# Performance work log

Measured on AMD Instinct MI355X. Metric: run time of the kernel, lower is better.

The kernel has to match this reference:

```python
import math
import jax, jax.numpy as jnp
import numpy as np

EMBED_DIM = 1024
NUM_HEADS = 16
FACTOR = 5


def setup_inputs() -> dict:
    key = jax.random.key(0)
    kx, kw, kb, kow, kob = jax.random.split(key, 5)
    B, S, E = 8, 4096, EMBED_DIM
    scale = 1.0 / math.sqrt(E)
    x = jax.random.normal(kx, (B, S, E), dtype=jnp.float32)
    # nn.MultiheadAttention params: packed in_proj (q,k,v) and out_proj
    in_proj_w = jax.random.uniform(kw, (3 * E, E), dtype=jnp.float32, minval=-scale, maxval=scale)
    in_proj_b = jnp.zeros((3 * E,), dtype=jnp.float32)
    out_w = jax.random.uniform(kow, (E, E), dtype=jnp.float32, minval=-scale, maxval=scale)
    out_b = jnp.zeros((E,), dtype=jnp.float32)
    return {"x": x, "in_proj_w": in_proj_w, "in_proj_b": in_proj_b, "out_w": out_w, "out_b": out_b}


def reference(x, in_proj_w, in_proj_b, out_w, out_b):
    B, S, E = x.shape
    H = NUM_HEADS
    hd = E // H
    k = max(1, int(FACTOR * math.log(S + 1)))
    k = min(k, S)

    # top-k queries by L2 norm of each token
    energy = jnp.linalg.norm(x, axis=-1)            # [B, S]
    _, topk_idx = jax.lax.top_k(energy, k)          # [B, k]

    q_tok = jnp.take_along_axis(x, topk_idx[..., None], axis=1)  # [B, k, E]

    Wq, Wk, Wv = jnp.split(in_proj_w, 3, axis=0)    # each [E, E]
    bq, bk, bv = jnp.split(in_proj_b, 3, axis=0)

    q = (q_tok @ Wq.T + bq).reshape(B, k, H, hd)    # [B, k, H, hd]
    kk = (x @ Wk.T + bk).reshape(B, S, H, hd)       # [B, S, H, hd]
    v = (x @ Wv.T + bv).reshape(B, S, H, hd)

    scores = jnp.einsum("bqhd,bshd->bhqs", q, kk) / math.sqrt(hd)
    attn = jax.nn.softmax(scores, axis=-1)          # [B, H, k, S]
    ctx = jnp.einsum("bhqs,bshd->bqhd", attn, v).reshape(B, k, E)
    out_sel = ctx @ out_w.T + out_b                 # [B, k, E]

    # default value for non-selected positions: per-batch mean of x
    default = jnp.mean(x, axis=1)                   # [B, E]
    result = jnp.broadcast_to(default[:, None, :], (B, S, E))
    batch_ar = jnp.arange(B)[:, None]
    result = result.at[batch_ar, topk_idx].set(out_sel)
    return result
```

## Files before the change

kernel.cpp:

```cpp
#include <hip/hip_runtime.h>

using u16 = unsigned short;
using u32 = unsigned int;
using u64 = unsigned long long;
typedef __attribute__((ext_vector_type(8))) short s16x8;
typedef __attribute__((ext_vector_type(4))) short s16x4;
typedef __attribute__((ext_vector_type(4))) float f32x4;

__device__ __forceinline__ float bf2f(u16 u){ return __uint_as_float(((u32)u)<<16); }
__device__ __forceinline__ u16 f2bf(float f){
  u32 u = __float_as_uint(f);
  u += 0x7fffu + ((u>>16)&1u);
  return (u16)(u>>16);
}
__device__ __forceinline__ void gl_lds16(const void* g, void* l){
  __builtin_amdgcn_global_load_lds((const __attribute__((address_space(1))) void*)g,
                                   (__attribute__((address_space(3))) void*)l, 16, 0, 0);
}

__global__ __launch_bounds__(256) void k_cvt(const float* __restrict__ in, u16* __restrict__ outp, int n){
  int i = (blockIdx.x*256 + threadIdx.x)*4;
  if (i >= n) return;
  float4 v = *(const float4*)(in + i);
  s16x4 o;
  o[0]=(short)f2bf(v.x); o[1]=(short)f2bf(v.y); o[2]=(short)f2bf(v.z); o[3]=(short)f2bf(v.w);
  *(s16x4*)(outp + i) = o;
}

__global__ __launch_bounds__(256) void k_prep_x(const float* __restrict__ x, u16* __restrict__ xb, float* __restrict__ energy){
  int tok = blockIdx.x*4 + (threadIdx.x>>6);
  int lane = threadIdx.x & 63;
  const float* p = x + (size_t)tok*1024 + lane*16;
  float4 a[4];
  #pragma unroll
  for (int j=0;j<4;++j) a[j] = ((const float4*)p)[j];
  float s = 0.f;
  s16x8 o0, o1;
  #pragma unroll
  for (int j=0;j<2;++j){
    o0[j*4+0]=(short)f2bf(a[j].x); o0[j*4+1]=(short)f2bf(a[j].y);
    o0[j*4+2]=(short)f2bf(a[j].z); o0[j*4+3]=(short)f2bf(a[j].w);
  }
  #pragma unroll
  for (int j=0;j<2;++j){
    o1[j*4+0]=(short)f2bf(a[2+j].x); o1[j*4+1]=(short)f2bf(a[2+j].y);
    o1[j*4+2]=(short)f2bf(a[2+j].z); o1[j*4+3]=(short)f2bf(a[2+j].w);
  }
  #pragma unroll
  for (int j=0;j<4;++j){
    s += a[j].x*a[j].x + a[j].y*a[j].y + a[j].z*a[j].z + a[j].w*a[j].w;
  }
  u16* xo = xb + (size_t)tok*1024 + lane*16;
  *(s16x8*)xo = o0;
  *(s16x8*)(xo+8) = o1;
  #pragma unroll
  for (int off=32; off; off>>=1) s += __shfl_xor(s, off);
  if (lane==0) energy[tok] = s;
}

__global__ __launch_bounds__(256) void k_colsum(const u16* __restrict__ xb, float* __restrict__ colsum){
  int b = blockIdx.x, sc = blockIdx.y;
  int t = threadIdx.x;
  float acc[4] = {0.f,0.f,0.f,0.f};
  for (int s = sc*128; s < sc*128+128; ++s){
    s16x4 v = *(const s16x4*)(xb + ((size_t)b*4096 + s)*1024 + t*4);
    #pragma unroll
    for (int i=0;i<4;++i) acc[i] += bf2f((u16)v[i]);
  }
  #pragma unroll
  for (int i=0;i<4;++i) atomicAdd(&colsum[b*1024 + t*4 + i], acc[i]);
}

__global__ __launch_bounds__(256) void k_topk(const float* __restrict__ energy, int* __restrict__ topk, int* __restrict__ sel){
  int b = blockIdx.x, t = threadIdx.x;
  int lane = t & 63, wid = t >> 6;
  __shared__ u64 wmax[4];
  __shared__ u64 winner;
  u64 v[16];
  #pragma unroll
  for (int i=0;i<16;++i){
    u32 tok = i*256 + t;
    float e = energy[b*4096 + tok];
    v[i] = ((u64)__float_as_uint(e) << 32) | (u32)(~tok);
    sel[b*4096 + tok] = -1;
  }
  __syncthreads();
  for (int it=0; it<41; ++it){
    u64 m = v[0];
    #pragma unroll
    for (int i=1;i<16;++i) m = v[i] > m ? v[i] : m;
    #pragma unroll
    for (int off=32; off; off>>=1){
      u64 o = __shfl_xor(m, off);
      m = o > m ? o : m;
    }
    if (lane==0) wmax[wid] = m;
    __syncthreads();
    if (t==0){
      u64 g = wmax[0];
      #pragma unroll
      for (int w=1;w<4;++w) g = wmax[w] > g ? wmax[w] : g;
      winner = g;
      u32 tok = (~(u32)g) & 4095u;
      topk[b*64+it] = (int)tok;
      sel[b*4096 + tok] = it;
    }
    __syncthreads();
    u32 wtok = (~(u32)winner) & 4095u;
    #pragma unroll
    for (int i=0;i<16;++i){
      if ((u32)(i*256 + t) == wtok) v[i] = 0;
    }
  }
}

__global__ __launch_bounds__(256) void k_gather_q(const float* __restrict__ x, const int* __restrict__ topk,
                                                  u16* __restrict__ Aq){
  int b = blockIdx.x, qi = blockIdx.y, t = threadIdx.x;
  size_t dst = ((size_t)(b*48+qi))*1024 + t*4;
  if (qi >= 41){ s16x4 z = {0,0,0,0}; *(s16x4*)&Aq[dst] = z; return; }
  int tok = topk[b*64+qi];
  float4 v = *(const float4*)(x + ((size_t)b*4096 + tok)*1024 + t*4);
  s16x4 o;
  o[0]=(short)f2bf(v.x); o[1]=(short)f2bf(v.y); o[2]=(short)f2bf(v.z); o[3]=(short)f2bf(v.w);
  *(s16x4*)&Aq[dst] = o;
}

__global__ __launch_bounds__(256) void k_gemm(const u16* __restrict__ A, const u16* __restrict__ Bk,
                                              const u16* __restrict__ Bv,
                                              const u16* __restrict__ biask, const u16* __restrict__ biasv,
                                              u16* __restrict__ C, int nbn, int ncols, int half, float cscale){
  __shared__ u16 As[128*64];
  __shared__ u16 Bs[128*64];
  const int tid = threadIdx.x;
  const int bn = blockIdx.x % nbn;
  const int bm = blockIdx.x / nbn;
  const int m0 = bm*128, n0 = bn*128;
  const u16* Bbase  = (n0 < half) ? (Bk + (size_t)n0*1024) : (Bv + (size_t)(n0-half)*1024);
  const u16* biasp  = (n0 < half) ? (biask + n0) : (biasv + (n0-half));
  const int lane = tid & 63;
  const int wave = tid >> 6;
  const int wr = wave >> 1, wc = wave & 1;
  const int fr = lane & 15;
  const int fq = lane >> 4;
  f32x4 acc[4][4] = {};
  for (int k0 = 0; k0 < 1024; k0 += 64){
    __syncthreads();
    #pragma unroll
    for (int j=0;j<4;++j){
      int idx = j*256 + tid;
      int r = idx>>3; int cc = (idx&7)*8;
      gl_lds16(A + (size_t)(m0+r)*1024 + k0 + cc, &As[r*64+cc]);
    }
    #pragma unroll
    for (int j=0;j<4;++j){
      int idx = j*256 + tid;
      int r = idx>>3; int cc = (idx&7)*8;
      gl_lds16(Bbase + (size_t)r*1024 + k0 + cc, &Bs[r*64+cc]);
    }
    __syncthreads();
    #pragma unroll
    for (int kk=0; kk<64; kk+=32){
      s16x8 af[4], bfv[4];
      #pragma unroll
      for (int m=0;m<4;++m) af[m] = *(const s16x8*)&As[(wr*64 + m*16 + fr)*64 + kk + fq*8];
      #pragma unroll
      for (int n=0;n<4;++n) bfv[n] = *(const s16x8*)&Bs[(wc*64 + n*16 + fr)*64 + kk + fq*8];
      #pragma unroll
      for (int m=0;m<4;++m)
        #pragma unroll
        for (int n=0;n<4;++n)
          acc[m][n] = __builtin_amdgcn_mfma_f32_16x16x32_bf16(af[m], bfv[n], acc[m][n], 0,0,0);
    }
  }
  #pragma unroll
  for (int n=0;n<4;++n){
    int cl = wc*64 + n*16 + fr;
    int col = n0 + cl;
    float bvv = bf2f(biasp[cl]);
    #pragma unroll
    for (int m=0;m<4;++m){
      int rowb = m0 + wr*64 + m*16 + fq*4;
      f32x4 v = acc[m][n];
      #pragma unroll
      for (int i=0;i<4;++i)
        C[(size_t)(rowb+i)*ncols + col] = f2bf((v[i]+bvv)*cscale);
    }
  }
}

__device__ __forceinline__ void stageA2(const u16* __restrict__ A, int m0, int k0, u16* ldsSlot, int tid){
  #pragma unroll
  for (int j=0;j<4;++j){
    int idx = j*512 + tid;
    int row = idx>>3;
    int chunk = (tid&7) ^ (row&7);
    gl_lds16(A + (size_t)(m0+row)*1024 + k0 + chunk*8, ldsSlot + (size_t)idx*8);
  }
}
__device__ __forceinline__ void stageB2(const u16* __restrict__ B, int k0, u16* ldsSlot, int tid){
  #pragma unroll
  for (int j=0;j<2;++j){
    int idx = j*512 + tid;
    int row = idx>>3;
    int chunk = (tid&7) ^ (row&7);
    gl_lds16(B + (size_t)row*1024 + k0 + chunk*8, ldsSlot + 16384 + (size_t)idx*8);
  }
}
__device__ __forceinline__ s16x8 fragA2(const u16* slot, int row, int k2, int fq){
  int chunk = (fq + k2*4) ^ (row&7);
  return *(const s16x8*)(slot + row*64 + chunk*8);
}
__device__ __forceinline__ s16x8 fragB2(const u16* slot, int row, int k2, int fq){
  int chunk = (fq + k2*4) ^ (row&7);
  return *(const s16x8*)(slot + 16384 + row*64 + chunk*8);
}

__global__ __launch_bounds__(512) void k_kvgemm2(const u16* __restrict__ A, const u16* __restrict__ Bk,
                                                 const u16* __restrict__ Bv,
                                                 const u16* __restrict__ biask, const u16* __restrict__ biasv,
                                                 u16* __restrict__ C){
  __shared__ u16 lds[3*24576];
  const int tid = threadIdx.x;
  const int bn = blockIdx.x & 15;
  const int bm = blockIdx.x >> 4;
  const int m0 = bm*256, n0 = bn*128;
  const u16* Bbase = (bn < 8) ? (Bk + (size_t)n0*1024) : (Bv + (size_t)(n0-1024)*1024);
  const u16* biasp = (bn < 8) ? (biask + n0) : (biasv + (n0-1024));
  const int lane = tid & 63, wid = tid >> 6;
  const int wm = wid >> 1, wn = wid & 1;
  const int fr = lane & 15, fq = lane >> 4;
  f32x4 acc[4][4] = {};

  stageA2(A, m0, 0, lds, tid);        stageB2(Bbase, 0, lds, tid);
  stageA2(A, m0, 64, lds+24576, tid); stageB2(Bbase, 64, lds+24576, tid);
  asm volatile("s_waitcnt vmcnt(6)" ::: "memory");
  __builtin_amdgcn_sched_barrier(0);
  __builtin_amdgcn_s_barrier();
  __builtin_amdgcn_sched_barrier(0);

  for (int t=0; t<16; ++t){
    const u16* slot = lds + (t%3)*24576;
    u16* nslot = (u16*)lds + ((t+2)%3)*24576;
    s16x8 afr[4][2], bfr[2][2];
    #pragma unroll
    for (int m=0;m<4;++m)
      #pragma unroll
      for (int k2=0;k2<2;++k2)
        afr[m][k2] = fragA2(slot, wm*64 + m*16 + fr, k2, fq);
    #pragma unroll
    for (int n=0;n<2;++n)
      #pragma unroll
      for (int k2=0;k2<2;++k2)
        bfr[n][k2] = fragB2(slot, wn*64 + n*16 + fr, k2, fq);
    if (t < 14) stageA2(A, m0, (t+2)*64, nslot, tid);
    __builtin_amdgcn_sched_barrier(0);
    __builtin_amdgcn_s_barrier();
    __builtin_amdgcn_sched_barrier(0);
    __builtin_amdgcn_s_setprio(1);
    #pragma unroll
    for (int m=0;m<4;++m)
      #pragma unroll
      for (int n=0;n<2;++n)
        #pragma unroll
        for (int k2=0;k2<2;++k2)
          acc[m][n] = __builtin_amdgcn_mfma_f32_16x16x32_bf16(afr[m][k2], bfr[n][k2], acc[m][n], 0,0,0);
    __builtin_amdgcn_s_setprio(0);
    __builtin_amdgcn_sched_barrier(0);
    __builtin_amdgcn_s_barrier();
    __builtin_amdgcn_sched_barrier(0);
    #pragma unroll
    for (int n=0;n<2;++n)
      #pragma unroll
      for (int k2=0;k2<2;++k2)
        bfr[n][k2] = fragB2(slot, wn*64 + (n+2)*16 + fr, k2, fq);
    if (t < 14) stageB2(Bbase, (t+2)*64, nslot, tid);
    __builtin_amdgcn_sched_barrier(0);
    __builtin_amdgcn_s_setprio(1);
    #pragma unroll
    for (int m=0;m<4;++m)
      #pragma unroll
      for (int n=0;n<2;++n)
        #pragma unroll
        for (int k2=0;k2<2;++k2)
          acc[m][n+2] = __builtin_amdgcn_mfma_f32_16x16x32_bf16(afr[m][k2], bfr[n][k2], acc[m][n+2], 0,0,0);
    __builtin_amdgcn_s_setprio(0);
    if (t < 14){
      asm volatile("s_waitcnt vmcnt(6)" ::: "memory");
    } else if (t == 14){
      asm volatile("s_waitcnt vmcnt(0)" ::: "memory");
    }
    __builtin_amdgcn_sched_barrier(0);
    __builtin_amdgcn_s_barrier();
    __builtin_amdgcn_sched_barrier(0);
  }

  #pragma unroll
  for (int n=0;n<4;++n){
    int cl = wn*64 + n*16 + fr;
    int col = n0 + cl;
    float bvv = bf2f(biasp[cl]);
    #pragma unroll
    for (int m=0;m<4;++m){
      int rowb = m0 + wm*64 + m*16 + fq*4;
      f32x4 v = acc[m][n];
      #pragma unroll
      for (int i=0;i<4;++i)
        C[(size_t)(rowb+i)*2048 + col] = f2bf(v[i]+bvv);
    }
  }
}

__global__ __launch_bounds__(64) void k_attn(const u16* __restrict__ qb, const u16* __restrict__ KV,
                                             float* __restrict__ part_ctx, float* __restrict__ part_ml,
                                             int G, int hg0, int ncols, int half, int nt, int NSP){
  const int b = blockIdx.x / G, hl = blockIdx.x % G;
  const int h = hg0 + hl;
  const int bh = b*16 + h;
  const int sp = blockIdx.y;
  const int lane = threadIdx.x;
  const int fr = lane & 15, fq = lane >> 4;
  __shared__ u16 k_lds[64*72];
  __shared__ u16 v_lds[64*72];
  __shared__ u16 p_lds[48*72];
  s16x8 af[3][2];
  #pragma unroll
  for (int m=0;m<3;++m)
    #pragma unroll
    for (int kk=0;kk<2;++kk)
      af[m][kk] = *(const s16x8*)(qb + ((size_t)(b*48 + m*16 + fr))*1024 + h*64 + kk*32 + fq*8);
  f32x4 acc_o[3][4] = {};
  float m_run[3][4], l_run[3][4];
  #pragma unroll
  for (int m=0;m<3;++m)
    #pragma unroll
    for (int i=0;i<4;++i){ m_run[m][i] = -3e38f; l_run[m][i] = 0.f; }

  for (int it=0; it<nt; ++it){
    int s0 = (sp*nt + it)*64;
    __syncthreads();
    #pragma unroll
    for (int j=0;j<8;++j){
      int r = j*8 + (lane>>3);
      int sg = (lane&7)*8;
      const u16* kp = KV + ((size_t)(b*4096 + s0 + r))*ncols + hl*64 + sg;
      *(s16x8*)&k_lds[r*72+sg] = *(const s16x8*)kp;
      *(s16x8*)&v_lds[r*72+sg] = *(const s16x8*)(kp+half);
    }
    __syncthreads();
    f32x4 sc4[3][4] = {};
    #pragma unroll
    for (int kk=0;kk<2;++kk){
      s16x8 bk[4];
      #pragma unroll
      for (int n=0;n<4;++n)
        bk[n] = *(const s16x8*)&k_lds[(n*16+fr)*72 + kk*32 + fq*8];
      #pragma unroll
      for (int m=0;m<3;++m)
        #pragma unroll
        for (int n=0;n<4;++n)
          sc4[m][n] = __builtin_amdgcn_mfma_f32_16x16x32_bf16(af[m][kk], bk[n], sc4[m][n], 0,0,0);
    }
    #pragma unroll
    for (int m=0;m<3;++m){
      #pragma unroll
      for (int i=0;i<4;++i){
        float rmax = fmaxf(fmaxf(sc4[m][0][i], sc4[m][1][i]), fmaxf(sc4[m][2][i], sc4[m][3][i]));
        #pragma unroll
        for (int off=1; off<16; off<<=1) rmax = fmaxf(rmax, __shfl_xor(rmax, off));
        float mnew = fmaxf(m_run[m][i], rmax);
        float alpha = __expf(m_run[m][i] - mnew);
        m_run[m][i] = mnew;
        float rsum = 0.f;
        #pragma unroll
        for (int n=0;n<4;++n){
          float p = __expf(sc4[m][n][i] - mnew);
          rsum += p;
          p_lds[(m*16 + fq*4 + i)*72 + n*16 + fr] = f2bf(p);
        }
        #pragma unroll
        for (int off=1; off<16; off<<=1) rsum += __shfl_xor(rsum, off);
        l_run[m][i] = l_run[m][i]*alpha + rsum;
        #pragma unroll
        for (int n=0;n<4;++n) acc_o[m][n][i] *= alpha;
      }
    }
    __syncthreads();
    #pragma unroll
    for (int kk=0;kk<2;++kk){
      s16x8 ap[3];
      #pragma unroll
      for (int m=0;m<3;++m)
        ap[m] = *(const s16x8*)&p_lds[(m*16+fr)*72 + kk*32 + fq*8];
      #pragma unroll
      for (int n=0;n<4;++n){
        s16x8 bv;
        #pragma unroll
        for (int i2=0;i2<8;++i2)
          bv[i2] = (short)v_lds[(kk*32 + fq*8 + i2)*72 + n*16 + fr];
        #pragma unroll
        for (int m=0;m<3;++m)
          acc_o[m][n] = __builtin_amdgcn_mfma_f32_16x16x32_bf16(ap[m], bv, acc_o[m][n], 0,0,0);
      }
    }
  }
  size_t pbase = ((size_t)(bh*NSP + sp))*48*64;
  #pragma unroll
  for (int m=0;m<3;++m)
    #pragma unroll
    for (int n=0;n<4;++n)
      #pragma unroll
      for (int i=0;i<4;++i){
        int qi = m*16 + fq*4 + i, d = n*16 + fr;
        part_ctx[pbase + (size_t)qi*64 + d] = acc_o[m][n][i];
      }
  if (fr==0){
    #pragma unroll
    for (int m=0;m<3;++m)
      #pragma unroll
      for (int i=0;i<4;++i){
        int qi = m*16 + fq*4 + i;
        part_ml[((size_t)(bh*NSP+sp))*96 + qi*2+0] = m_run[m][i];
        part_ml[((size_t)(bh*NSP+sp))*96 + qi*2+1] = l_run[m][i];
      }
  }
}

__global__ __launch_bounds__(64) void k_combine(const float* __restrict__ part_ctx, const float* __restrict__ part_ml,
                                                u16* __restrict__ ctxb, int NSP){
  int bh = blockIdx.x, qi = blockIdx.y;
  int b = bh>>4, h = bh&15;
  int lane = threadIdx.x;
  size_t dst = ((size_t)(b*48+qi))*1024 + h*64 + lane;
  if (qi >= 41){ ctxb[dst] = 0; return; }
  float M = -3e38f;
  for (int p=0;p<NSP;++p)
    M = fmaxf(M, part_ml[((size_t)(bh*NSP+p))*96 + qi*2+0]);
  float l = 0.f, c = 0.f;
  for (int p=0;p<NSP;++p){
    float pm = part_ml[((size_t)(bh*NSP+p))*96 + qi*2+0];
    float pl = part_ml[((size_t)(bh*NSP+p))*96 + qi*2+1];
    float w = __expf(pm-M);
    l += pl*w;
    c += w * part_ctx[((size_t)(bh*NSP+p))*48*64 + (size_t)qi*64 + lane];
  }
  ctxb[dst] = f2bf(c / l);
}

__global__ __launch_bounds__(256) void k_outscatter(const u16* __restrict__ outg, const int* __restrict__ topk,
                                                    float* __restrict__ out){
  int b = blockIdx.x, qi = blockIdx.y, t = threadIdx.x;
  int tok = topk[b*64+qi];
  s16x4 v = *(const s16x4*)&outg[((size_t)(b*48+qi))*1024 + t*4];
  float4 o;
  o.x = bf2f((u16)v[0]); o.y = bf2f((u16)v[1]); o.z = bf2f((u16)v[2]); o.w = bf2f((u16)v[3]);
  *(float4*)(out + ((size_t)b*4096 + tok)*1024 + t*4) = o;
}

__global__ __launch_bounds__(256) void k_meanfill(const float* __restrict__ colsum, const int* __restrict__ sel,
                                                  float* __restrict__ out){
  int row = blockIdx.x;
  if (sel[row] >= 0) return;
  int b = row >> 12;
  int t = threadIdx.x;
  float4 c = *(const float4*)(colsum + b*1024 + t*4);
  c.x *= (1.f/4096.f); c.y *= (1.f/4096.f); c.z *= (1.f/4096.f); c.w *= (1.f/4096.f);
  *(float4*)(out + (size_t)row*1024 + t*4) = c;
}

extern "C" void kernel_launch(void* const* d_in, const int* in_sizes, int n_in,
                              void* d_out, int out_size, void* d_ws, size_t ws_size,
                              hipStream_t stream) {
  const float* x    = (const float*)d_in[0];
  const float* ipw  = (const float*)d_in[1];
  const float* ipb  = (const float*)d_in[2];
  const float* outw = (const float*)d_in[3];
  const float* outb = (const float*)d_in[4];
  float* out = (float*)d_out;
  char* ws = (char*)d_ws;

  const int cfgG[7]   = {16, 8, 4, 2, 1, 1, 1};
  const int cfgNSP[7] = {16,16,16,16,16, 4, 2};
  int G = 1, NSP = 2;
  size_t oXB=0,oWIP=0,oBIP=0,oWO=0,oBO=0,oEN=0,oCS=0,oTK=0,oSEL=0,oAQ=0,oQB=0,oCTXB=0,oOG=0,oPML=0,oPCTX=0,oKV=0;
  for (int ci=0; ci<7; ++ci){
    int g = cfgG[ci], nsp = cfgNSP[ci];
    size_t o = 0;
    size_t xb=o;   o += 67108864;
    size_t wip=o;  o += 6291456;
    size_t bip=o;  o += 6144;
    size_t wo=o;   o += 2097152;
    size_t bo=o;   o += 2048;
    size_t en=o;   o += 131072;
    size_t cs=o;   o += 32768;
    size_t tk=o;   o += 2048;
    size_t sl=o;   o += 131072;
    size_t aq=o;   o += 786432;
    size_t qb=o;   o += 786432;
    size_t cb=o;   o += 786432;
    size_t og=o;   o += 786432;
    size_t pm=o;   o += (size_t)nsp*49152;
    size_t pc=o;   o += (size_t)nsp*1572864;
    size_t kv=o;   o += (size_t)g*8388608;
    if (o <= ws_size || ci == 6){
      G=g; NSP=nsp;
      oXB=xb; oWIP=wip; oBIP=bip; oWO=wo; oBO=bo; oEN=en; oCS=cs; oTK=tk; oSEL=sl;
      oAQ=aq; oQB=qb; oCTXB=cb; oOG=og; oPML=pm; oPCTX=pc; oKV=kv;
      break;
    }
  }

  u16*   xb     = (u16*)(ws + oXB);
  u16*   ipwb   = (u16*)(ws + oWIP);
  u16*   ipbb   = (u16*)(ws + oBIP);
  u16*   outwb  = (u16*)(ws + oWO);
  u16*   outbb  = (u16*)(ws + oBO);
  float* energy = (float*)(ws + oEN);
  float* colsum = (float*)(ws + oCS);
  int*   topk   = (int*)(ws + oTK);
  int*   sel    = (int*)(ws + oSEL);
  u16*   Aq     = (u16*)(ws + oAQ);
  u16*   qbf    = (u16*)(ws + oQB);
  u16*   ctxb   = (u16*)(ws + oCTXB);
  u16*   outg   = (u16*)(ws + oOG);
  float* pml    = (float*)(ws + oPML);
  float* pctx   = (float*)(ws + oPCTX);
  u16*   KV     = (u16*)(ws + oKV);

  hipMemsetAsync(colsum, 0, 8*1024*sizeof(float), stream);

  k_cvt <<<3072, 256, 0, stream>>>(ipw,  ipwb,  3145728);
  k_cvt <<<   3, 256, 0, stream>>>(ipb,  ipbb,  3072);
  k_cvt <<<1024, 256, 0, stream>>>(outw, outwb, 1048576);
  k_cvt <<<   1, 256, 0, stream>>>(outb, outbb, 1024);

  k_prep_x <<<8192, 256, 0, stream>>>(x, xb, energy);
  k_colsum <<<dim3(8,32), 256, 0, stream>>>(xb, colsum);
  k_topk   <<<8, 256, 0, stream>>>(energy, topk, sel);
  k_gather_q<<<dim3(8,48), 256, 0, stream>>>(x, topk, Aq);

  k_gemm <<<24, 256, 0, stream>>>(Aq, ipwb, ipwb, ipbb, ipbb, qbf, 8, 1024, 1024, 0.125f);

  if (G == 16){
    const int nt = 64/NSP;
    k_kvgemm2 <<<2048, 512, 0, stream>>>(xb,
        ipwb + (size_t)1024*1024, ipwb + (size_t)2048*1024,
        ipbb + 1024, ipbb + 2048, KV);
    k_attn <<<dim3(128, NSP), 64, 0, stream>>>(qbf, KV, pctx, pml, 16, 0, 2048, 1024, nt, NSP);
  } else {
    const int nchunk = 16 / G;
    const int ncols = G*128, half = G*64, nt = 64/NSP;
    for (int c=0; c<nchunk; ++c){
      int hg0 = c*G;
      k_gemm <<<G*256, 256, 0, stream>>>(
          xb,
          ipwb + (size_t)(1024 + hg0*64)*1024,
          ipwb + (size_t)(2048 + hg0*64)*1024,
          ipbb + 1024 + hg0*64,
          ipbb + 2048 + hg0*64,
          KV, G, ncols, half, 1.0f);
      k_attn <<<dim3(8*G, NSP), 64, 0, stream>>>(qbf, KV, pctx, pml, G, hg0, ncols, half, nt, NSP);
    }
  }

  k_combine<<<dim3(128,48), 64, 0, stream>>>(pctx, pml, ctxb, NSP);

  k_gemm <<<24, 256, 0, stream>>>(ctxb, outwb, outwb, outbb, outbb, outg, 8, 1024, 1024, 1.0f);

  k_outscatter<<<dim3(8,41), 256, 0, stream>>>(outg, topk, out);
  k_meanfill  <<<32768, 256, 0, stream>>>(colsum, sel, out);
}
```

Measured before the change: 431.6 us.

## Fuse conversion and finalize kernels, remap KV GEMM blocks, simplify pipeline

Merges the four weight-conversion launches into one kernel and merges the output scatter and mean-fill into a single finalize kernel that writes every output row once. In the KV GEMM it remaps block indices so that consecutive blocks share column tiles across XCDs. It also removes the split-phase barriers, issuing both next-stage loads up front and doing all MFMAs in one phase. This cuts launch overhead and barrier stalls, but the simpler schedule may overlap loads with compute less well and holds more registers for the larger B fragment array.

```diff
diff --git a/kernel.cpp b/kernel.cpp
--- a/kernel.cpp
+++ b/kernel.cpp
@@ -18,13 +18,22 @@
                                    (__attribute__((address_space(3))) void*)l, 16, 0, 0);
 }
 
-__global__ __launch_bounds__(256) void k_cvt(const float* __restrict__ in, u16* __restrict__ outp, int n){
-  int i = (blockIdx.x*256 + threadIdx.x)*4;
+__global__ __launch_bounds__(256) void k_cvt_all(const float* __restrict__ ipw, const float* __restrict__ ipb,
+                                                 const float* __restrict__ outw, const float* __restrict__ outb,
+                                                 u16* __restrict__ ipwb, u16* __restrict__ ipbb,
+                                                 u16* __restrict__ outwb, u16* __restrict__ outbb){
+  int bid = blockIdx.x;
+  const float* src; u16* dst; int n; int base;
+  if (bid < 3072){ src=ipw; dst=ipwb; n=3145728; base=bid; }
+  else if (bid < 3075){ src=ipb; dst=ipbb; n=3072; base=bid-3072; }
+  else if (bid < 4099){ src=outw; dst=outwb; n=1048576; base=bid-3075; }
+  else { src=outb; dst=outbb; n=1024; base=0; }
+  int i = (base*256 + threadIdx.x)*4;
   if (i >= n) return;
-  float4 v = *(const float4*)(in + i);
+  float4 v = *(const float4*)(src + i);
   s16x4 o;
   o[0]=(short)f2bf(v.x); o[1]=(short)f2bf(v.y); o[2]=(short)f2bf(v.z); o[3]=(short)f2bf(v.w);
-  *(s16x4*)(outp + i) = o;
+  *(s16x4*)(dst + i) = o;
 }
 
 __global__ __launch_bounds__(256) void k_prep_x(const float* __restrict__ x, u16* __restrict__ xb, float* __restrict__ energy){
@@ -222,8 +231,9 @@
                                                  u16* __restrict__ C){
   __shared__ u16 lds[3*24576];
   const int tid = threadIdx.x;
-  const int bn = blockIdx.x & 15;
-  const int bm = blockIdx.x >> 4;
+  const int sbid = (blockIdx.x & 7)*256 + (blockIdx.x >> 3);
+  const int bn = sbid & 15;
+  const int bm = sbid >> 4;
   const int m0 = bm*256, n0 = bn*128;
   const u16* Bbase = (bn < 8) ? (Bk + (size_t)n0*1024) : (Bv + (size_t)(n0-1024)*1024);
   const u16* biasp = (bn < 8) ? (biask + n0) : (biasv + (n0-1024));
@@ -235,64 +245,38 @@
   stageA2(A, m0, 0, lds, tid);        stageB2(Bbase, 0, lds, tid);
   stageA2(A, m0, 64, lds+24576, tid); stageB2(Bbase, 64, lds+24576, tid);
   asm volatile("s_waitcnt vmcnt(6)" ::: "memory");
-  __builtin_amdgcn_sched_barrier(0);
   __builtin_amdgcn_s_barrier();
-  __builtin_amdgcn_sched_barrier(0);
 
   for (int t=0; t<16; ++t){
     const u16* slot = lds + (t%3)*24576;
     u16* nslot = (u16*)lds + ((t+2)%3)*24576;
-    s16x8 afr[4][2], bfr[2][2];
+    if (t < 14){ stageA2(A, m0, (t+2)*64, nslot, tid); stageB2(Bbase, (t+2)*64, nslot, tid); }
+    s16x8 afr[4][2], bfr[4][2];
     #pragma unroll
     for (int m=0;m<4;++m)
       #pragma unroll
       for (int k2=0;k2<2;++k2)
         afr[m][k2] = fragA2(slot, wm*64 + m*16 + fr, k2, fq);
     #pragma unroll
-    for (int n=0;n<2;++n)
+    for (int n=0;n<4;++n)
       #pragma unroll
       for (int k2=0;k2<2;++k2)
         bfr[n][k2] = fragB2(slot, wn*64 + n*16 + fr, k2, fq);
-    if (t < 14) stageA2(A, m0, (t+2)*64, nslot, tid);
-    __builtin_amdgcn_sched_barrier(0);
-    __builtin_amdgcn_s_barrier();
-    __builtin_amdgcn_sched_barrier(0);
     __builtin_amdgcn_s_setprio(1);
     #pragma unroll
     for (int m=0;m<4;++m)
       #pragma unroll
-      for (int n=0;n<2;++n)
+      for (int n=0;n<4;++n)
         #pragma unroll
         for (int k2=0;k2<2;++k2)
           acc[m][n] = __builtin_amdgcn_mfma_f32_16x16x32_bf16(afr[m][k2], bfr[n][k2], acc[m][n], 0,0,0);
-    __builtin_amdgcn_s_setprio(0);
-    __builtin_amdgcn_sched_barrier(0);
-    __builtin_amdgcn_s_barrier();
-    __builtin_amdgcn_sched_barrier(0);
-    #pragma unroll
-    for (int n=0;n<2;++n)
-      #pragma unroll
-      for (int k2=0;k2<2;++k2)
-        bfr[n][k2] = fragB2(slot, wn*64 + (n+2)*16 + fr, k2, fq);
-    if (t < 14) stageB2(Bbase, (t+2)*64, nslot, tid);
-    __builtin_amdgcn_sched_barrier(0);
-    __builtin_amdgcn_s_setprio(1);
-    #pragma unroll
-    for (int m=0;m<4;++m)
-      #pragma unroll
-      for (int n=0;n<2;++n)
-        #pragma unroll
-        for (int k2=0;k2<2;++k2)
-          acc[m][n+2] = __builtin_amdgcn_mfma_f32_16x16x32_bf16(afr[m][k2], bfr[n][k2], acc[m][n+2], 0,0,0);
     __builtin_amdgcn_s_setprio(0);
     if (t < 14){
       asm volatile("s_waitcnt vmcnt(6)" ::: "memory");
     } else if (t == 14){
       asm volatile("s_waitcnt vmcnt(0)" ::: "memory");
     }
-    __builtin_amdgcn_sched_barrier(0);
     __builtin_amdgcn_s_barrier();
-    __builtin_amdgcn_sched_barrier(0);
   }
 
   #pragma unroll
@@ -447,25 +431,21 @@
   ctxb[dst] = f2bf(c / l);
 }
 
-__global__ __launch_bounds__(256) void k_outscatter(const u16* __restrict__ outg, const int* __restrict__ topk,
-                                                    float* __restrict__ out){
-  int b = blockIdx.x, qi = blockIdx.y, t = threadIdx.x;
-  int tok = topk[b*64+qi];
-  s16x4 v = *(const s16x4*)&outg[((size_t)(b*48+qi))*1024 + t*4];
-  float4 o;
-  o.x = bf2f((u16)v[0]); o.y = bf2f((u16)v[1]); o.z = bf2f((u16)v[2]); o.w = bf2f((u16)v[3]);
-  *(float4*)(out + ((size_t)b*4096 + tok)*1024 + t*4) = o;
-}
-
-__global__ __launch_bounds__(256) void k_meanfill(const float* __restrict__ colsum, const int* __restrict__ sel,
-                                                  float* __restrict__ out){
+__global__ __launch_bounds__(256) void k_finalize(const u16* __restrict__ outg, const float* __restrict__ colsum,
+                                                  const int* __restrict__ sel, float* __restrict__ out){
   int row = blockIdx.x;
-  if (sel[row] >= 0) return;
   int b = row >> 12;
   int t = threadIdx.x;
-  float4 c = *(const float4*)(colsum + b*1024 + t*4);
-  c.x *= (1.f/4096.f); c.y *= (1.f/4096.f); c.z *= (1.f/4096.f); c.w *= (1.f/4096.f);
-  *(float4*)(out + (size_t)row*1024 + t*4) = c;
+  int s = sel[row];
+  float4 o;
+  if (s >= 0){
+    s16x4 v = *(const s16x4*)&outg[((size_t)(b*48+s))*1024 + t*4];
+    o.x = bf2f((u16)v[0]); o.y = bf2f((u16)v[1]); o.z = bf2f((u16)v[2]); o.w = bf2f((u16)v[3]);
+  } else {
+    o = *(const float4*)(colsum + b*1024 + t*4);
+    o.x *= (1.f/4096.f); o.y *= (1.f/4096.f); o.z *= (1.f/4096.f); o.w *= (1.f/4096.f);
+  }
+  *(float4*)(out + (size_t)row*1024 + t*4) = o;
 }
 
 extern "C" void kernel_launch(void* const* d_in, const int* in_sizes, int n_in,
@@ -529,10 +509,7 @@
 
   hipMemsetAsync(colsum, 0, 8*1024*sizeof(float), stream);
 
-  k_cvt <<<3072, 256, 0, stream>>>(ipw,  ipwb,  3145728);
-  k_cvt <<<   3, 256, 0, stream>>>(ipb,  ipbb,  3072);
-  k_cvt <<<1024, 256, 0, stream>>>(outw, outwb, 1048576);
-  k_cvt <<<   1, 256, 0, stream>>>(outb, outbb, 1024);
+  k_cvt_all <<<4100, 256, 0, stream>>>(ipw, ipb, outw, outb, ipwb, ipbb, outwb, outbb);
 
   k_prep_x <<<8192, 256, 0, stream>>>(x, xb, energy);
   k_colsum <<<dim3(8,32), 256, 0, stream>>>(xb, colsum);
@@ -567,6 +544,5 @@
 
   k_gemm <<<24, 256, 0, stream>>>(ctxb, outwb, outwb, outbb, outbb, outg, 8, 1024, 1024, 1.0f);
 
-  k_outscatter<<<dim3(8,41), 256, 0, stream>>>(outg, topk, out);
-  k_meanfill  <<<32768, 256, 0, stream>>>(colsum, sel, out);
-}
+  k_finalize<<<32768, 256, 0, stream>>>(outg, colsum, sel, out);
+}
```

Result: faster. 413.9 us (-4.1%).
